# Kernel tuning notes

Hardware: AMD Instinct MI355X
Metric: run time of the kernel (lower is better)

Reference implementation:

```python
import jax, jax.numpy as jnp
import numpy as np

B, LATENT, H, OUT, T, L = 4096, 128, 256, 88, 64, 5  # batch, latent, hidden, output(88 keys), seq_len, num_layers


def setup_inputs() -> dict:
    key = jax.random.key(0)
    ks = jax.random.split(key, 8)
    sc = 1.0 / np.sqrt(H)
    n = lambda k, shp, s: (jax.random.normal(k, shp, jnp.float32) * s)
    return {
        "x": jax.random.normal(ks[0], (B, LATENT), jnp.float32),
        "linear_w": n(ks[1], (H, LATENT), 1.0 / np.sqrt(LATENT)),
        "linear_b": jnp.zeros((H,), jnp.float32),
        # PyTorch LSTM layout: [4H, in] with gate order i, f, g, o. Layer-0 input size == H.
        "w_ih": n(ks[2], (L, 4 * H, H), sc),
        "w_hh": n(ks[3], (L, 4 * H, H), sc),
        "b_ih": n(ks[4], (L, 4 * H), sc),
        "b_hh": n(ks[5], (L, 4 * H), sc),
        "out_w": n(ks[6], (OUT, H), sc),
        "out_b": jnp.zeros((OUT,), jnp.float32),
    }


def _lstm_cell(gates, c):
    # gates: [B, 4H] pre-activation, PyTorch order i, f, g, o
    i, f, g, o = jnp.split(gates, 4, axis=-1)
    c_new = jax.nn.sigmoid(f) * c + jax.nn.sigmoid(i) * jnp.tanh(g)
    h_new = jax.nn.sigmoid(o) * jnp.tanh(c_new)
    return h_new, c_new


def _lstm(xp, w_ih, w_hh, b_ih, b_hh):
    # xp: [B, H] latent projection, repeated over T timesteps (constant input).
    bsz = xp.shape[0]
    gx0 = xp @ w_ih[0].T + b_ih[0]  # layer-0 input gates, constant across time [B, 4H]
    h0 = jnp.zeros((L, bsz, H), xp.dtype)
    c0 = jnp.zeros((L, bsz, H), xp.dtype)

    def step(carry, _):
        h, c = carry  # [L, B, H]
        hs, cs = [], []
        layer_in_gates = gx0
        for l in range(L):  # fixed small loop over structurally distinct layers
            if l > 0:
                layer_in_gates = hs[-1] @ w_ih[l].T + b_ih[l]
            gates = layer_in_gates + h[l] @ w_hh[l].T + b_hh[l]
            hl, cl = _lstm_cell(gates, c[l])
            hs.append(hl)
            cs.append(cl)
        return (jnp.stack(hs), jnp.stack(cs)), hs[-1]

    _, ys = jax.lax.scan(step, (h0, c0), None, length=T)  # ys: [T, B, H]
    return ys.transpose(1, 0, 2)  # [B, T, H]


def reference(x, linear_w, linear_b, w_ih, w_hh, b_ih, b_hh, out_w, out_b):
    xp = x @ linear_w.T + linear_b  # [B, H]; unsqueeze+repeat folded into constant gx0
    y = _lstm(xp, w_ih, w_hh, b_ih, b_hh)  # [B, T, H]
    return jax.nn.sigmoid(y @ out_w.T + out_b)  # [B, T, OUT]
```

## Files before the change

### kernel.cpp

```cpp
#include <hip/hip_runtime.h>
#include <hip/hip_bf16.h>
#include <cstdint>

#define B_ 4096
#define H_ 256
#define G_ 1024
#define T_ 64
#define L_ 5

typedef __hip_bfloat16 bf16;
typedef __bf16 bf16x8 __attribute__((ext_vector_type(8)));
typedef float f32x4 __attribute__((ext_vector_type(4)));

#define OFF_WCOMB   0ull
#define OFF_WIH0R   5242880ull
#define OFF_LWB     5767168ull
#define OFF_XB      5832704ull
#define OFF_OBW     6881280ull
#define OFF_BIAS    6930432ull
#define OFF_XP      6950912ull
#define OFF_GX0     9048064ull
#define OFF_H0      25825280ull
#define OFF_H1      34213888ull
#define OFF_C1      42602496ull
#define OFF_YS      63574016ull
#define OFF_C0      199888896ull
#define TOTAL_WS    220860416ull
#define ZERO_BYTES  31457280ull
#define SLOT_H      2097152ull
#define SLOT_C      4194304ull

__device__ __forceinline__ bf16* h_ptr(char* ws, int l, int p) {
  return (bf16*)(ws + (p ? OFF_H1 : OFF_H0) + (size_t)l * SLOT_H);
}
__device__ __forceinline__ float* c_ptr(char* ws, int l, int p) {
  return (float*)(ws + (p ? OFF_C1 : OFF_C0) + (size_t)l * SLOT_C);
}
__device__ __forceinline__ bf16* ys_ptr(char* ws, int s) {
  return (bf16*)(ws + OFF_YS + (size_t)s * SLOT_H);
}

__device__ __forceinline__ float frcp(float x) { return __builtin_amdgcn_rcpf(x); }
__device__ __forceinline__ float fsig(float x) { return frcp(1.0f + __expf(-x)); }
__device__ __forceinline__ float ftanh(float x) { return 1.0f - 2.0f * frcp(1.0f + __expf(2.0f * x)); }

__device__ __forceinline__ void gload16(const void* g, void* l) {
  __builtin_amdgcn_global_load_lds((const __attribute__((address_space(1))) void*)g,
                                   (__attribute__((address_space(3))) void*)l, 16, 0, 0);
}

__device__ __forceinline__ void stage_tile(char* dst, const bf16* src, long stride, int koff,
                                           int wv, int lane) {
#pragma unroll
  for (int i = 0; i < 4; ++i) {
    int r = 32 * wv + 8 * i + (lane >> 3);
    int cb = ((lane & 7) << 4) ^ ((r & 7) << 4);
    const bf16* g = src + (long)r * stride + koff + (cb >> 1);
    char* ld = dst + (32 * wv + 8 * i) * 128;
    gload16(g, ld);
  }
}

template <int OUTMODE>
__device__ void gemm_core(const bf16* __restrict__ A1, int lda1,
                          const bf16* __restrict__ A2,
                          const bf16* __restrict__ W, int ldw, int K,
                          const float* __restrict__ bias,
                          const float* __restrict__ acc2d,
                          float* __restrict__ outF, bf16* __restrict__ outB, int ldo,
                          const float* __restrict__ cIn, float* __restrict__ cOut,
                          bf16* __restrict__ hOut,
                          int mtile, int ntile, char* smem) {
  const int tid = threadIdx.x;
  const int lane = tid & 63, wv = tid >> 6;
  const int wrow = wv >> 1, wcol = wv & 1;
  const int row0 = mtile * 128;
  const int n0 = ntile * 128;

  char* As[2] = { smem,          smem + 16384 };
  char* Bs[2] = { smem + 32768,  smem + 49152 };

  f32x4 acc[4][4];
  if (acc2d) {
#pragma unroll
    for (int m = 0; m < 4; m++)
#pragma unroll
      for (int n = 0; n < 4; n++)
#pragma unroll
        for (int r = 0; r < 4; r++) {
          int row = row0 + wrow * 64 + 16 * m + ((lane >> 4) << 2) + r;
          int col = n0 + wcol * 64 + 16 * n + (lane & 15);
          acc[m][n][r] = acc2d[(long)row * G_ + col];
        }
  } else {
#pragma unroll
    for (int n = 0; n < 4; n++) {
      int col = n0 + wcol * 64 + 16 * n + (lane & 15);
      float bv = bias ? bias[col] : 0.0f;
#pragma unroll
      for (int m = 0; m < 4; m++)
#pragma unroll
        for (int r = 0; r < 4; r++) acc[m][n][r] = bv;
    }
  }

  const int nkb = K >> 6;
  {
    const bf16* s = A1 + (long)row0 * lda1;
    stage_tile(As[0], s, lda1, 0, wv, lane);
    stage_tile(Bs[0], W + (long)n0 * ldw, ldw, 0, wv, lane);
  }
  for (int kb = 0; kb < nkb; ++kb) {
    __syncthreads();
    if (kb + 1 < nkb) {
      int k2 = kb + 1, b = k2 & 1;
      if (k2 < 4) stage_tile(As[b], A1 + (long)row0 * lda1, lda1, k2 * 64, wv, lane);
      else        stage_tile(As[b], A2 + (long)row0 * 256,  256,  k2 * 64 - 256, wv, lane);
      stage_tile(Bs[b], W + (long)n0 * ldw, ldw, k2 * 64, wv, lane);
    }
    char* Ab = As[kb & 1]; char* Bb = Bs[kb & 1];
#pragma unroll
    for (int ks = 0; ks < 2; ++ks) {
      bf16x8 af[4], bfr[4];
#pragma unroll
      for (int m = 0; m < 4; m++) {
        int r = wrow * 64 + 16 * m + (lane & 15);
        int cb = (ks * 64 + ((lane >> 4) << 4)) ^ ((r & 7) << 4);
        af[m] = *(const bf16x8*)(Ab + r * 128 + cb);
      }
#pragma unroll
      for (int n = 0; n < 4; n++) {
        int r = wcol * 64 + 16 * n + (lane & 15);
        int cb = (ks * 64 + ((lane >> 4) << 4)) ^ ((r & 7) << 4);
        bfr[n] = *(const bf16x8*)(Bb + r * 128 + cb);
      }
#pragma unroll
      for (int m = 0; m < 4; m++)
#pragma unroll
        for (int n = 0; n < 4; n++)
          acc[m][n] = __builtin_amdgcn_mfma_f32_16x16x32_bf16(af[m], bfr[n], acc[m][n], 0, 0, 0);
    }
  }
  __syncthreads();

  if (OUTMODE == 0 || OUTMODE == 1) {
#pragma unroll
    for (int m = 0; m < 4; m++)
#pragma unroll
      for (int n = 0; n < 4; n++)
#pragma unroll
        for (int r = 0; r < 4; r++) {
          int row = row0 + wrow * 64 + 16 * m + ((lane >> 4) << 2) + r;
          int col = n0 + wcol * 64 + 16 * n + (lane & 15);
          if (OUTMODE == 0) outF[(long)row * ldo + col] = acc[m][n][r];
          else              outB[(long)row * ldo + col] = __float2bfloat16(acc[m][n][r]);
        }
  } else {
#pragma unroll
    for (int m = 0; m < 4; m++)
#pragma unroll
      for (int n = 0; n < 4; n++)
#pragma unroll
        for (int r = 0; r < 4; r++) {
          int rr = wrow * 64 + 16 * m + ((lane >> 4) << 2) + r;
          int cc = wcol * 64 + 16 * n + (lane & 15);
          int byte = (rr << 9) + (((cc << 2)) ^ ((rr & 7) << 4));
          *(float*)(smem + byte) = acc[m][n][r];
        }
    __syncthreads();
    int j = tid & 31;
    int rbase = tid >> 5;
#pragma unroll
    for (int i = 0; i < 16; i++) {
      int rr = rbase + 8 * i;
      int byte = (rr << 9) + ((j << 4) ^ ((rr & 7) << 4));
      f32x4 g4 = *(const f32x4*)(smem + byte);
      int row = row0 + rr;
      int jj = ntile * 32 + j;
      float cold = cIn[(long)row * H_ + jj];
      float cn = fsig(g4[1]) * cold + fsig(g4[0]) * ftanh(g4[2]);
      float hn = fsig(g4[3]) * ftanh(cn);
      cOut[(long)row * H_ + jj] = cn;
      hOut[(long)row * H_ + jj] = __float2bfloat16(hn);
    }
  }
}

template <int OUTMODE>
__global__ __launch_bounds__(256) void gemm_generic(const bf16* A1, int lda1,
                                                    const bf16* W, int ldw, int K,
                                                    const float* bias,
                                                    float* outF, bf16* outB, int ldo) {
  __shared__ __align__(16) char smem[65536];
  int mtile = blockIdx.x & 31;
  int ntile = blockIdx.x >> 5;
  gemm_core<OUTMODE>(A1, lda1, A1 , W, ldw, K, bias, nullptr,
                     outF, outB, ldo, nullptr, nullptr, nullptr, mtile, ntile, smem);
}

__global__ __launch_bounds__(256) void lstm_diag(int d, char* __restrict__ ws) {
  __shared__ __align__(16) char smem[65536];
  int l0 = d > 63 ? d - 63 : 0;
  int l = l0 + blockIdx.y;
  int t = d - l;
  int mtile = blockIdx.x & 31;
  int ntile = blockIdx.x >> 5;
  int sp = (t & 1) ^ 1, op = t & 1;

  const bf16* wc = (const bf16*)(ws + OFF_WCOMB) + (long)l * G_ * 512;
  const bf16* A1; const bf16* A2 = nullptr; int K;
  const float* bias = nullptr; const float* acc2d = nullptr;
  if (l == 0) {
    A1 = h_ptr(ws, 0, sp); A2 = A1; K = 256;
    acc2d = (const float*)(ws + OFF_GX0);
  } else {
    A1 = h_ptr(ws, l - 1, op);
    A2 = (l == 4) ? ys_ptr(ws, t) : h_ptr(ws, l, sp);
    K = 512;
    bias = (const float*)(ws + OFF_BIAS) + l * G_;
  }
  const float* cIn = c_ptr(ws, l, sp);
  float* cOut = c_ptr(ws, l, op);
  bf16* hOut = (l == 4) ? ys_ptr(ws, t + 1) : h_ptr(ws, l, op);

  gemm_core<2>(A1, 256, A2, wc, 512, K, bias, acc2d,
               nullptr, nullptr, 0, cIn, cOut, hOut, mtile, ntile, smem);
}

__global__ __launch_bounds__(256) void proj_kernel(char* __restrict__ ws,
                                                   const float* __restrict__ ob,
                                                   float* __restrict__ out) {
  __shared__ __align__(16) char smem[49152];
  int mtile = blockIdx.x;
  int t = blockIdx.y;
  const bf16* ys = ys_ptr(ws, t + 1);
  const char* obw = (const char*)(ws + OFF_OBW);
  int tid = threadIdx.x, lane = tid & 63, wv = tid >> 6;
#pragma unroll
  for (int i = 0; i < 12; i++) {
    int r = wv * 24 + i * 2 + (lane >> 5);
    int cb = ((lane & 31) << 4) ^ ((r & 7) << 4);
    gload16(obw + r * 512 + cb, smem + (wv * 24 + i * 2) * 512);
  }
  __syncthreads();
  f32x4 acc[2][6];
#pragma unroll
  for (int m = 0; m < 2; m++)
#pragma unroll
    for (int n = 0; n < 6; n++)
#pragma unroll
      for (int r = 0; r < 4; r++) acc[m][n][r] = 0.0f;
  const char* arow = (const char*)(ys + (long)(mtile * 128) * 256);
  for (int kk = 0; kk < 256; kk += 32) {
    bf16x8 af[2], bfr[6];
#pragma unroll
    for (int m = 0; m < 2; m++) {
      int r = wv * 32 + 16 * m + (lane & 15);
      af[m] = *(const bf16x8*)(arow + (long)r * 512 + kk * 2 + ((lane >> 4) << 4));
    }
#pragma unroll
    for (int n = 0; n < 6; n++) {
      int r = 16 * n + (lane & 15);
      int cb = (kk * 2 + ((lane >> 4) << 4)) ^ ((r & 7) << 4);
      bfr[n] = *(const bf16x8*)(smem + r * 512 + cb);
    }
#pragma unroll
    for (int m = 0; m < 2; m++)
#pragma unroll
      for (int n = 0; n < 6; n++)
        acc[m][n] = __builtin_amdgcn_mfma_f32_16x16x32_bf16(af[m], bfr[n], acc[m][n], 0, 0, 0);
  }
#pragma unroll
  for (int m = 0; m < 2; m++)
#pragma unroll
    for (int n = 0; n < 6; n++)
#pragma unroll
      for (int r = 0; r < 4; r++) {
        int row = mtile * 128 + wv * 32 + 16 * m + ((lane >> 4) << 2) + r;
        int o = 16 * n + (lane & 15);
        if (o < 88) {
          float v = acc[m][n][r] + ob[o];
          out[((long)row * T_ + t) * 88 + o] = fsig(v);
        }
      }
}

__global__ void prep_kernel(const float* __restrict__ x, const float* __restrict__ lw,
                            const float* __restrict__ wih, const float* __restrict__ whh,
                            const float* __restrict__ bih, const float* __restrict__ bhh,
                            const float* __restrict__ ow, char* __restrict__ ws) {
  bf16* xb = (bf16*)(ws + OFF_XB);
  bf16* lwb = (bf16*)(ws + OFF_LWB);
  bf16* wcomb = (bf16*)(ws + OFF_WCOMB);
  bf16* wih0r = (bf16*)(ws + OFF_WIH0R);
  bf16* obw = (bf16*)(ws + OFF_OBW);
  float* bias = (float*)(ws + OFF_BIAS);
  const int S0 = 524288, S1 = 32768, S2 = 2621440, S3 = 262144, S4 = 24576, S5 = 5120;
  const int total = S0 + S1 + S2 + S3 + S4 + S5;
  for (int i = blockIdx.x * blockDim.x + threadIdx.x; i < total; i += gridDim.x * blockDim.x) {
    int idx = i;
    if (idx < S0) { xb[idx] = __float2bfloat16(x[idx]); continue; }
    idx -= S0;
    if (idx < S1) { lwb[idx] = __float2bfloat16(lw[idx]); continue; }
    idx -= S1;
    if (idx < S2) {
      int l = idx >> 19;
      int rem = idx & 524287;
      int n = rem >> 9;
      int k = rem & 511;
      int row = (n & 3) * 256 + (n >> 2);
      float v;
      if (l == 0) v = (k < 256) ? whh[row * 256 + k] : 0.0f;
      else        v = (k < 256) ? wih[(l * 1024 + row) * 256 + k]
                                : whh[(l * 1024 + row) * 256 + (k - 256)];
      wcomb[idx] = __float2bfloat16(v); continue;
    }
    idx -= S2;
    if (idx < S3) {
      int n = idx >> 8, k = idx & 255;
      int row = (n & 3) * 256 + (n >> 2);
      wih0r[idx] = __float2bfloat16(wih[row * 256 + k]); continue;
    }
    idx -= S3;
    if (idx < S4) {
      int r = idx >> 8, k = idx & 255;
      obw[idx] = __float2bfloat16(r < 88 ? ow[r * 256 + k] : 0.0f); continue;
    }
    idx -= S4;
    {
      int l = idx >> 10, n = idx & 1023;
      int row = (n & 3) * 256 + (n >> 2);
      bias[idx] = bih[l * 1024 + row] + bhh[l * 1024 + row];
    }
  }
}

extern "C" void kernel_launch(void* const* d_in, const int* in_sizes, int n_in,
                              void* d_out, int out_size, void* d_ws, size_t ws_size,
                              hipStream_t stream) {
  const float* x   = (const float*)d_in[0];
  const float* lw  = (const float*)d_in[1];
  const float* lb  = (const float*)d_in[2];
  const float* wih = (const float*)d_in[3];
  const float* whh = (const float*)d_in[4];
  const float* bih = (const float*)d_in[5];
  const float* bhh = (const float*)d_in[6];
  const float* ow  = (const float*)d_in[7];
  const float* ob  = (const float*)d_in[8];
  char* ws = (char*)d_ws;
  float* out = (float*)d_out;

  if (ws_size < TOTAL_WS) return;

  hipMemsetAsync(ws + OFF_H1, 0, ZERO_BYTES, stream);
  prep_kernel<<<2048, 256, 0, stream>>>(x, lw, wih, whh, bih, bhh, ow, ws);

  gemm_generic<1><<<dim3(64), 256, 0, stream>>>(
      (const bf16*)(ws + OFF_XB), 128, (const bf16*)(ws + OFF_LWB), 128, 128,
      lb, nullptr, (bf16*)(ws + OFF_XP), 256);

  gemm_generic<0><<<dim3(256), 256, 0, stream>>>(
      (const bf16*)(ws + OFF_XP), 256, (const bf16*)(ws + OFF_WIH0R), 256, 256,
      (const float*)(ws + OFF_BIAS), (float*)(ws + OFF_GX0), nullptr, 1024);

  for (int d = 0; d < 68; ++d) {
    int lo = d > 63 ? d - 63 : 0;
    int hi = d < 4 ? d : 4;
    int nc = hi - lo + 1;
    lstm_diag<<<dim3(256, nc), 256, 0, stream>>>(d, ws);
  }

  proj_kernel<<<dim3(32, 64), 256, 0, stream>>>(ws, ob, out);
}
```

Measured before the change: 2.427 ms.

## Halve LDS with single-buffered tiles, split epilogue, skip zero-state work at t=0

Drops the double-buffered LDS staging for a single buffer, cutting shared memory from 64KB to 32KB so more workgroups can be resident per CU. The LSTM epilogue is split into two column halves so the gate transpose fits in the smaller buffer. At t=0 the zero hidden-state part of the GEMM and the cell-state read are skipped, which removes the workspace memset. Blocks are also remapped so neighbouring workgroups share tiles for better cache reuse. The cost is the loss of load/compute overlap, since every k-step now stalls on its global loads.

```diff
diff --git a/kernel.cpp b/kernel.cpp
--- a/kernel.cpp
+++ b/kernel.cpp
@@ -26,7 +26,6 @@
 #define OFF_YS      63574016ull
 #define OFF_C0      199888896ull
 #define TOTAL_WS    220860416ull
-#define ZERO_BYTES  31457280ull
 #define SLOT_H      2097152ull
 #define SLOT_C      4194304ull
 
@@ -77,8 +76,8 @@
   const int row0 = mtile * 128;
   const int n0 = ntile * 128;
 
-  char* As[2] = { smem,          smem + 16384 };
-  char* Bs[2] = { smem + 32768,  smem + 49152 };
+  char* As = smem;
+  char* Bs = smem + 16384;
 
   f32x4 acc[4][4];
   if (acc2d) {
@@ -105,20 +104,11 @@
   }
 
   const int nkb = K >> 6;
-  {
-    const bf16* s = A1 + (long)row0 * lda1;
-    stage_tile(As[0], s, lda1, 0, wv, lane);
-    stage_tile(Bs[0], W + (long)n0 * ldw, ldw, 0, wv, lane);
-  }
   for (int kb = 0; kb < nkb; ++kb) {
+    if (kb < 4) stage_tile(As, A1 + (long)row0 * lda1, lda1, kb * 64, wv, lane);
+    else        stage_tile(As, A2 + (long)row0 * 256,  256,  kb * 64 - 256, wv, lane);
+    stage_tile(Bs, W + (long)n0 * ldw, ldw, kb * 64, wv, lane);
     __syncthreads();
-    if (kb + 1 < nkb) {
-      int k2 = kb + 1, b = k2 & 1;
-      if (k2 < 4) stage_tile(As[b], A1 + (long)row0 * lda1, lda1, k2 * 64, wv, lane);
-      else        stage_tile(As[b], A2 + (long)row0 * 256,  256,  k2 * 64 - 256, wv, lane);
-      stage_tile(Bs[b], W + (long)n0 * ldw, ldw, k2 * 64, wv, lane);
-    }
-    char* Ab = As[kb & 1]; char* Bb = Bs[kb & 1];
 #pragma unroll
     for (int ks = 0; ks < 2; ++ks) {
       bf16x8 af[4], bfr[4];
@@ -126,13 +116,13 @@
       for (int m = 0; m < 4; m++) {
         int r = wrow * 64 + 16 * m + (lane & 15);
         int cb = (ks * 64 + ((lane >> 4) << 4)) ^ ((r & 7) << 4);
-        af[m] = *(const bf16x8*)(Ab + r * 128 + cb);
+        af[m] = *(const bf16x8*)(As + r * 128 + cb);
       }
 #pragma unroll
       for (int n = 0; n < 4; n++) {
         int r = wcol * 64 + 16 * n + (lane & 15);
         int cb = (ks * 64 + ((lane >> 4) << 4)) ^ ((r & 7) << 4);
-        bfr[n] = *(const bf16x8*)(Bb + r * 128 + cb);
+        bfr[n] = *(const bf16x8*)(Bs + r * 128 + cb);
       }
 #pragma unroll
       for (int m = 0; m < 4; m++)
@@ -140,8 +130,8 @@
         for (int n = 0; n < 4; n++)
           acc[m][n] = __builtin_amdgcn_mfma_f32_16x16x32_bf16(af[m], bfr[n], acc[m][n], 0, 0, 0);
     }
-  }
-  __syncthreads();
+    __syncthreads();
+  }
 
   if (OUTMODE == 0 || OUTMODE == 1) {
 #pragma unroll
@@ -157,31 +147,35 @@
         }
   } else {
 #pragma unroll
-    for (int m = 0; m < 4; m++)
-#pragma unroll
-      for (int n = 0; n < 4; n++)
-#pragma unroll
-        for (int r = 0; r < 4; r++) {
-          int rr = wrow * 64 + 16 * m + ((lane >> 4) << 2) + r;
-          int cc = wcol * 64 + 16 * n + (lane & 15);
-          int byte = (rr << 9) + (((cc << 2)) ^ ((rr & 7) << 4));
-          *(float*)(smem + byte) = acc[m][n][r];
-        }
-    __syncthreads();
-    int j = tid & 31;
-    int rbase = tid >> 5;
-#pragma unroll
-    for (int i = 0; i < 16; i++) {
-      int rr = rbase + 8 * i;
-      int byte = (rr << 9) + ((j << 4) ^ ((rr & 7) << 4));
-      f32x4 g4 = *(const f32x4*)(smem + byte);
-      int row = row0 + rr;
-      int jj = ntile * 32 + j;
-      float cold = cIn[(long)row * H_ + jj];
-      float cn = fsig(g4[1]) * cold + fsig(g4[0]) * ftanh(g4[2]);
-      float hn = fsig(g4[3]) * ftanh(cn);
-      cOut[(long)row * H_ + jj] = cn;
-      hOut[(long)row * H_ + jj] = __float2bfloat16(hn);
+    for (int h = 0; h < 2; ++h) {
+      if (wcol == h) {
+#pragma unroll
+        for (int m = 0; m < 4; m++)
+#pragma unroll
+          for (int n = 0; n < 4; n++)
+#pragma unroll
+            for (int r = 0; r < 4; r++) {
+              int rr = wrow * 64 + 16 * m + ((lane >> 4) << 2) + r;
+              int cc2 = 16 * n + (lane & 15);
+              *(float*)(smem + rr * 256 + ((cc2 << 2) ^ ((rr & 7) << 4))) = acc[m][n][r];
+            }
+      }
+      __syncthreads();
+      int j2 = tid & 15;
+      int rb = tid >> 4;
+#pragma unroll
+      for (int i = 0; i < 8; i++) {
+        int rr = rb + 16 * i;
+        f32x4 g4 = *(const f32x4*)(smem + rr * 256 + ((j2 << 4) ^ ((rr & 7) << 4)));
+        int row = row0 + rr;
+        int jj = ntile * 32 + 16 * h + j2;
+        float cold = cIn ? cIn[(long)row * H_ + jj] : 0.0f;
+        float cn = fsig(g4[1]) * cold + fsig(g4[0]) * ftanh(g4[2]);
+        float hn = fsig(g4[3]) * ftanh(cn);
+        cOut[(long)row * H_ + jj] = cn;
+        hOut[(long)row * H_ + jj] = __float2bfloat16(hn);
+      }
+      if (h == 0) __syncthreads();
     }
   }
 }
@@ -191,7 +185,7 @@
                                                     const bf16* W, int ldw, int K,
                                                     const float* bias,
                                                     float* outF, bf16* outB, int ldo) {
-  __shared__ __align__(16) char smem[65536];
+  __shared__ __align__(16) char smem[32768];
   int mtile = blockIdx.x & 31;
   int ntile = blockIdx.x >> 5;
   gemm_core<OUTMODE>(A1, lda1, A1 , W, ldw, K, bias, nullptr,
@@ -199,27 +193,32 @@
 }
 
 __global__ __launch_bounds__(256) void lstm_diag(int d, char* __restrict__ ws) {
-  __shared__ __align__(16) char smem[65536];
+  __shared__ __align__(16) char smem[32768];
   int l0 = d > 63 ? d - 63 : 0;
   int l = l0 + blockIdx.y;
   int t = d - l;
-  int mtile = blockIdx.x & 31;
-  int ntile = blockIdx.x >> 5;
+  int bid = blockIdx.x;
+  int wg = (bid & 7) * 32 + (bid >> 3);
+  int w = wg & 31, q = wg >> 5;
+  int mtile = q * 4 + (w & 3);
+  int ntile = w >> 2;
   int sp = (t & 1) ^ 1, op = t & 1;
+  bool tz = (t == 0);
 
   const bf16* wc = (const bf16*)(ws + OFF_WCOMB) + (long)l * G_ * 512;
-  const bf16* A1; const bf16* A2 = nullptr; int K;
+  const bf16* A1; const bf16* A2; int K;
   const float* bias = nullptr; const float* acc2d = nullptr;
   if (l == 0) {
-    A1 = h_ptr(ws, 0, sp); A2 = A1; K = 256;
+    A1 = h_ptr(ws, 0, sp); A2 = A1;
+    K = tz ? 0 : 256;
     acc2d = (const float*)(ws + OFF_GX0);
   } else {
     A1 = h_ptr(ws, l - 1, op);
     A2 = (l == 4) ? ys_ptr(ws, t) : h_ptr(ws, l, sp);
-    K = 512;
+    K = tz ? 256 : 512;
     bias = (const float*)(ws + OFF_BIAS) + l * G_;
   }
-  const float* cIn = c_ptr(ws, l, sp);
+  const float* cIn = tz ? nullptr : c_ptr(ws, l, sp);
   float* cOut = c_ptr(ws, l, op);
   bf16* hOut = (l == 4) ? ys_ptr(ws, t + 1) : h_ptr(ws, l, op);
 
@@ -352,7 +351,6 @@
 
   if (ws_size < TOTAL_WS) return;
 
-  hipMemsetAsync(ws + OFF_H1, 0, ZERO_BYTES, stream);
   prep_kernel<<<2048, 256, 0, stream>>>(x, lw, wih, whh, bih, bhh, ow, ws);
 
   gemm_generic<1><<<dim3(64), 256, 0, stream>>>(
```

New measurement: 2.987 ms. 23.1% more time.

## Store gate accumulators and cell state in tile-native fragment layout

Applied to the files above, without the earlier changes.

Stores the fp32 GX0 accumulator buffer and the LSTM cell state in a per-tile layout that follows the MFMA fragment and thread ownership. Each thread then reads and writes them with contiguous 16-byte vector accesses instead of strided scalar accesses. This targets memory transactions in the recurrent step and the gate precompute. It depends on every producer and consumer of these buffers agreeing on the new layout. The hidden code must also handle any zero initialisation or other uses accordingly.

```diff
diff --git a/kernel.cpp b/kernel.cpp
--- a/kernel.cpp
+++ b/kernel.cpp
@@ -76,22 +76,18 @@
   const int wrow = wv >> 1, wcol = wv & 1;
   const int row0 = mtile * 128;
   const int n0 = ntile * 128;
+  const int tile_id = mtile * 8 + ntile;
 
   char* As[2] = { smem,          smem + 16384 };
   char* Bs[2] = { smem + 32768,  smem + 49152 };
 
   f32x4 acc[4][4];
   if (acc2d) {
+    const f32x4* g4 = (const f32x4*)acc2d + (((long)tile_id) << 12) + tid * 16;
 #pragma unroll
     for (int m = 0; m < 4; m++)
 #pragma unroll
-      for (int n = 0; n < 4; n++)
-#pragma unroll
-        for (int r = 0; r < 4; r++) {
-          int row = row0 + wrow * 64 + 16 * m + ((lane >> 4) << 2) + r;
-          int col = n0 + wcol * 64 + 16 * n + (lane & 15);
-          acc[m][n][r] = acc2d[(long)row * G_ + col];
-        }
+      for (int n = 0; n < 4; n++) acc[m][n] = g4[m * 4 + n];
   } else {
 #pragma unroll
     for (int n = 0; n < 4; n++) {
@@ -143,7 +139,13 @@
   }
   __syncthreads();
 
-  if (OUTMODE == 0 || OUTMODE == 1) {
+  if (OUTMODE == 0) {
+    f32x4* o4 = (f32x4*)outF + (((long)tile_id) << 12) + tid * 16;
+#pragma unroll
+    for (int m = 0; m < 4; m++)
+#pragma unroll
+      for (int n = 0; n < 4; n++) o4[m * 4 + n] = acc[m][n];
+  } else if (OUTMODE == 1) {
 #pragma unroll
     for (int m = 0; m < 4; m++)
 #pragma unroll
@@ -152,8 +154,7 @@
         for (int r = 0; r < 4; r++) {
           int row = row0 + wrow * 64 + 16 * m + ((lane >> 4) << 2) + r;
           int col = n0 + wcol * 64 + 16 * n + (lane & 15);
-          if (OUTMODE == 0) outF[(long)row * ldo + col] = acc[m][n][r];
-          else              outB[(long)row * ldo + col] = __float2bfloat16(acc[m][n][r]);
+          outB[(long)row * ldo + col] = __float2bfloat16(acc[m][n][r]);
         }
   } else {
 #pragma unroll
@@ -170,6 +171,12 @@
     __syncthreads();
     int j = tid & 31;
     int rbase = tid >> 5;
+    const f32x4* cin4 = (const f32x4*)cIn + (((long)tile_id) << 10) + tid * 4;
+    f32x4* cout4 = (f32x4*)cOut + (((long)tile_id) << 10) + tid * 4;
+    f32x4 cv[4];
+#pragma unroll
+    for (int q = 0; q < 4; q++) cv[q] = cin4[q];
+    f32x4 cn4[4];
 #pragma unroll
     for (int i = 0; i < 16; i++) {
       int rr = rbase + 8 * i;
@@ -177,12 +184,14 @@
       f32x4 g4 = *(const f32x4*)(smem + byte);
       int row = row0 + rr;
       int jj = ntile * 32 + j;
-      float cold = cIn[(long)row * H_ + jj];
+      float cold = cv[i >> 2][i & 3];
       float cn = fsig(g4[1]) * cold + fsig(g4[0]) * ftanh(g4[2]);
       float hn = fsig(g4[3]) * ftanh(cn);
-      cOut[(long)row * H_ + jj] = cn;
+      cn4[i >> 2][i & 3] = cn;
       hOut[(long)row * H_ + jj] = __float2bfloat16(hn);
     }
+#pragma unroll
+    for (int q = 0; q < 4; q++) cout4[q] = cn4[q];
   }
 }
 
```

After: 2.637 ms. +8.7%, slower.
